# Kernel tuning notes

Hardware: AMD Instinct MI355X
Metric: run time of the kernel (lower is better)

## Reference

```python
import jax, jax.numpy as jnp
import numpy as np

UNITS = 32
OUT_STEPS = 24
B, T, F = 131072, 48, 1


def setup_inputs() -> dict:
    key = jax.random.key(0)
    ks = jax.random.split(key, 9)
    s = 0.1
    return {
        "inputs": jax.random.normal(ks[0], (B, T, F), jnp.float32),
        # warmup LSTM cell (inside lstm_rnn_warmup)
        "Wk_w": jax.random.normal(ks[1], (F, 4 * UNITS), jnp.float32) * s,
        "Uk_w": jax.random.normal(ks[2], (UNITS, 4 * UNITS), jnp.float32) * s,
        "b_w": jax.random.normal(ks[3], (4 * UNITS,), jnp.float32) * s,
        # decode LSTM cell (self.lstm_cell), input dim = 1 (prediction)
        "Wk_d": jax.random.normal(ks[4], (1, 4 * UNITS), jnp.float32) * s,
        "Uk_d": jax.random.normal(ks[5], (UNITS, 4 * UNITS), jnp.float32) * s,
        "b_d": jax.random.normal(ks[6], (4 * UNITS,), jnp.float32) * s,
        # dense projection to 1 output
        "Wd": jax.random.normal(ks[7], (UNITS, 1), jnp.float32) * s,
        "bd": jax.random.normal(ks[8], (1,), jnp.float32) * s,
    }


def _lstm_cell(x, h, c, Wk, Uk, b):
    # Keras LSTMCell: z = x@W + h@U + b ; split into i,f,g,o
    z = x @ Wk + h @ Uk + b
    i, f, g, o = jnp.split(z, 4, axis=-1)
    i = jax.nn.sigmoid(i)
    f = jax.nn.sigmoid(f)
    g = jnp.tanh(g)
    o = jax.nn.sigmoid(o)
    c_new = f * c + i * g
    h_new = o * jnp.tanh(c_new)
    return h_new, c_new


def reference(inputs, Wk_w, Uk_w, b_w, Wk_d, Uk_d, b_d, Wd, bd):
    b = inputs.shape[0]
    h0 = jnp.zeros((b, UNITS), inputs.dtype)
    c0 = jnp.zeros((b, UNITS), inputs.dtype)

    # warmup: run LSTM over input window, keep final state
    def warm_step(carry, x_t):
        h, c = carry
        h, c = _lstm_cell(x_t, h, c, Wk_w, Uk_w, b_w)
        return (h, c), None

    (h, c), _ = jax.lax.scan(warm_step, (h0, c0), jnp.swapaxes(inputs, 0, 1))
    pred = h @ Wd + bd  # [B, 1]

    def dec_step(carry, _):
        h, c, p = carry
        h, c = _lstm_cell(p, h, c, Wk_d, Uk_d, b_d)
        p = h @ Wd + bd
        return (h, c, p), p

    _, preds_rest = jax.lax.scan(dec_step, (h, c, pred), None, length=OUT_STEPS - 1)
    preds = jnp.concatenate([pred[None], preds_rest], axis=0)  # [S, B, 1]
    return jnp.transpose(preds, (1, 0, 2))  # [B, S, 1]
```

## Files before the change

kernel.cpp:

```cpp
#include <hip/hip_runtime.h>

#define TSTEPS 48
#define OUT_STEPS 24
#define L2E 1.44269504088896340736f
#define ECLAMP 30.0f

typedef short bf16x8 __attribute__((ext_vector_type(8)));
typedef float f32x16 __attribute__((ext_vector_type(16)));
typedef float f32x4 __attribute__((ext_vector_type(4)));
typedef unsigned int u32x4 __attribute__((ext_vector_type(4)));

__device__ __forceinline__ void bf_split_rne(float f, short& hi, short& lo) {
    unsigned u = __builtin_bit_cast(unsigned, f);
    unsigned r = u + 0x7FFFu + ((u >> 16) & 1u);
    unsigned short hb = (unsigned short)(r >> 16);
    float hif = __builtin_bit_cast(float, (unsigned)hb << 16);
    float lof = f - hif;
    unsigned short lb = (unsigned short)(__builtin_bit_cast(unsigned, lof) >> 16);
    hi = (short)hb; lo = (short)lb;
}

__device__ __forceinline__ float gate_scale(int g) {
    return (g == 2) ? (-2.0f * L2E) : (-L2E);
}

__device__ __forceinline__ int uslot(int cell, int g, int c) {
    return (cell * 4 + g) * 2 + c;
}

__device__ __forceinline__ void stage_a4(short* __restrict__ a4lds,
                                         const float* __restrict__ Wks,
                                         const float* __restrict__ bvs,
                                         int m, int H, int lane) {
#pragma unroll
    for (int g = 0; g < 4; ++g) {
        const float s = gate_scale(g);
        short whi, wlo, bhi, blo;
        bf_split_rne(Wks[g * 32 + m] * s, whi, wlo);
        bf_split_rne(bvs[g * 32 + m] * s, bhi, blo);
        bf16x8 a = {whi, wlo, bhi, blo, 0, 0, 0, 0};
        u32x4 z4 = {0u, 0u, 0u, 0u};
        if (H != 0) a = __builtin_bit_cast(bf16x8, z4);
        *(bf16x8*)(a4lds + (g * 64 + lane) * 8) = a;
    }
}

template <bool NEED_P>
__device__ __forceinline__ float lstm_step32(float x,
    const short* __restrict__ ufbase,
    const short* __restrict__ a4cell,
    u32x4& B0, u32x4& B1,
    float* cs, const float* __restrict__ wdp,
    int lane, unsigned hmask) {
    unsigned xr;
    asm("v_cvt_pk_bf16_f32 %0, %1, %2" : "=v"(xr) : "v"(x), "v"(x));
    unsigned w0 = xr & hmask;
    unsigned w1 = 0x3F803F80u & hmask;
    u32x4 b4u = {w0, w1, 0u, 0u};
    const bf16x8 B4 = __builtin_bit_cast(bf16x8, b4u);
    const bf16x8 b0 = __builtin_bit_cast(bf16x8, B0);
    const bf16x8 b1 = __builtin_bit_cast(bf16x8, B1);
    const f32x16 zero16 = {0,0,0,0,0,0,0,0,0,0,0,0,0,0,0,0};

    f32x16 acc[4];
#pragma unroll
    for (int g = 0; g < 4; ++g) {
        const bf16x8 A4g = *(const bf16x8*)(a4cell + (g * 64 + lane) * 8);
        const bf16x8 Ah0 = *(const bf16x8*)(ufbase + (uslot(0, g, 0) * 64 + lane) * 8);
        const bf16x8 Ah1 = *(const bf16x8*)(ufbase + (uslot(0, g, 1) * 64 + lane) * 8);
        f32x16 a = __builtin_amdgcn_mfma_f32_32x32x16_bf16(A4g, B4, zero16, 0, 0, 0);
        a = __builtin_amdgcn_mfma_f32_32x32x16_bf16(Ah0, b0, a, 0, 0, 0);
        a = __builtin_amdgcn_mfma_f32_32x32x16_bf16(Ah1, b1, a, 0, 0, 0);
        acc[g] = a;
    }

    float pp = 0.0f;
    float he = 0.0f;
    f32x4 wq = {0.0f, 0.0f, 0.0f, 0.0f};
#pragma unroll
    for (int r = 0; r < 16; ++r) {
        float ei = __builtin_amdgcn_exp2f(acc[0][r]);
        float ef = __builtin_amdgcn_exp2f(acc[1][r]);
        float eg = __builtin_amdgcn_exp2f(acc[2][r]);
        float eo = __builtin_amdgcn_exp2f(acc[3][r]);
        float di = 1.0f + ei, df = 1.0f + ef, dg = 1.0f + eg, do_ = 1.0f + eo;
        float ngs = __builtin_fmaf(eg, 2.0f * L2E, -2.0f * L2E);
        float t1 = di * dg;
        float t2 = cs[r] * t1;
        float num = __builtin_fmaf(ngs, df, t2);
        float cn = num * __builtin_amdgcn_rcpf(df * t1);
        cs[r] = cn;
        float ec = __builtin_amdgcn_exp2f(__builtin_fminf(cn, ECLAMP));
        float den = __builtin_fmaf(ec, do_, do_);
        float inv = __builtin_amdgcn_rcpf(den);
        float h = __builtin_fmaf(-ec, inv, inv);
        if constexpr (NEED_P) {
            if ((r & 3) == 0) wq = *(const f32x4*)(wdp + r);
            pp = __builtin_fmaf(h, wq[r & 3], pp);
        }
        if ((r & 1) == 0) {
            he = h;
        } else {
            unsigned d;
            asm("v_cvt_pk_bf16_f32 %0, %1, %2" : "=v"(d) : "v"(he), "v"(h));
            const int q = r >> 1;
            if (q < 4) B0[q] = d;
            else       B1[q - 4] = d;
        }
    }
    return pp;
}

__global__ __launch_bounds__(256, 4) void lstm_feedback_mfma22(
    const float* __restrict__ inputs,
    const float* __restrict__ Wk_w, const float* __restrict__ Uk_w, const float* __restrict__ b_w,
    const float* __restrict__ Wk_d, const float* __restrict__ Uk_d, const float* __restrict__ b_d,
    const float* __restrict__ Wd, const float* __restrict__ bd,
    float* __restrict__ out,
    int B) {
    const int tid = threadIdx.x;
    const int w = tid >> 6;
    const int lane = tid & 63;
    const int m = lane & 31;
    const int H = lane >> 5;
    const int mblk = blockIdx.x * 128;
    const long row = (long)(mblk + w * 32 + m);

    __shared__ __align__(16) short uflds[16 * 64 * 8];
    __shared__ __align__(16) short a4lds[4 * 64 * 8];
    __shared__ float wdlds[2][16];

    if (w < 2) {
        const float* Uks = w ? Uk_d : Uk_w;
#pragma unroll
        for (int g = 0; g < 4; ++g) {
            const float s = gate_scale(g);
#pragma unroll
            for (int c = 0; c < 2; ++c) {
                bf16x8 ah;
#pragma unroll
                for (int j = 0; j < 8; ++j) {
                    const int uin = 16 * c + 4 * H + (j & 3) + 8 * (j >> 2);
                    float wt = Uks[uin * 128 + g * 32 + m] * s;
                    short hb, lb; bf_split_rne(wt, hb, lb);
                    ah[j] = hb;
                }
                *(bf16x8*)(uflds + (uslot(w, g, c) * 64 + lane) * 8) = ah;
            }
        }
    }
    if (w == 0) stage_a4(a4lds, Wk_w, b_w, m, H, lane);
    if (tid < 32) {
        const int r = tid & 15, Hh = tid >> 4;
        wdlds[Hh][r] = Wd[(r & 3) + 8 * (r >> 2) + 4 * Hh];
    }

    const unsigned hmask = (H == 0) ? 0xFFFFFFFFu : 0u;

    u32x4 z4 = {0u, 0u, 0u, 0u};
    u32x4 B0 = z4, B1 = z4;
    float cs[16];
#pragma unroll
    for (int r = 0; r < 16; ++r) cs[r] = 0.0f;

    __syncthreads();

    const short* __restrict__ uf_w = uflds;
    const short* __restrict__ uf_d = uflds + 8 * 64 * 8;
    const float* __restrict__ wdp = &wdlds[H][0];

    float xc = inputs[row * TSTEPS + 0];
    for (int t = 0; t < TSTEPS - 1; ++t) {
        float xn = inputs[row * TSTEPS + t + 1];
        asm volatile("" ::: "memory");
        lstm_step32<false>(xc, uf_w, a4lds, B0, B1, cs, wdp, lane, hmask);
        xc = xn;
    }

    const float bdv = bd[0];

    asm volatile("" ::: "memory");
    float p = lstm_step32<true>(xc, uf_w, a4lds, B0, B1, cs, wdp, lane, hmask);
    p += __shfl_xor(p, 32);
    p += bdv;
    if (H == 0) out[row * OUT_STEPS + 0] = p;

    __syncthreads();
    if (w == 0) stage_a4(a4lds, Wk_d, b_d, m, H, lane);
    __syncthreads();

    for (int s = 1; s < OUT_STEPS; ++s) {
        asm volatile("" ::: "memory");
        p = lstm_step32<true>(p, uf_d, a4lds, B0, B1, cs, wdp, lane, hmask);
        p += __shfl_xor(p, 32);
        p += bdv;
        if (H == 0) out[row * OUT_STEPS + s] = p;
    }
}

extern "C" void kernel_launch(void* const* d_in, const int* in_sizes, int n_in,
                              void* d_out, int out_size, void* d_ws, size_t ws_size,
                              hipStream_t stream) {
    const float* inputs = (const float*)d_in[0];
    const float* Wk_w   = (const float*)d_in[1];
    const float* Uk_w   = (const float*)d_in[2];
    const float* b_w    = (const float*)d_in[3];
    const float* Wk_d   = (const float*)d_in[4];
    const float* Uk_d   = (const float*)d_in[5];
    const float* b_d    = (const float*)d_in[6];
    const float* Wd     = (const float*)d_in[7];
    const float* bd     = (const float*)d_in[8];
    float* out = (float*)d_out;

    const int B = in_sizes[0] / TSTEPS;
    const int grid = (B + 127) / 128;
    lstm_feedback_mfma22<<<grid, 256, 0, stream>>>(
        inputs, Wk_w, Uk_w, b_w, Wk_d, Uk_d, b_d, Wd, bd, out, B);
}
```

Measured before the change: 318.2 us.

## Keep LSTM weight fragments and Wd in registers instead of LDS

Loads the recurrent weight MFMA fragments, the input/bias fragment, and the dense-projection weights into per-thread registers once per phase, instead of re-reading them from shared memory every timestep. The launch bounds drop from 4 to 2 waves per SIMD so the extra registers fit, and the per-step compiler memory barriers are removed. This cuts per-step LDS read traffic and latency in exchange for fewer resident waves to hide MFMA and transcendental latency.

```diff
diff --git a/kernel.cpp b/kernel.cpp
--- a/kernel.cpp
+++ b/kernel.cpp
@@ -28,10 +28,9 @@
     return (cell * 4 + g) * 2 + c;
 }
 
-__device__ __forceinline__ void stage_a4(short* __restrict__ a4lds,
-                                         const float* __restrict__ Wks,
-                                         const float* __restrict__ bvs,
-                                         int m, int H, int lane) {
+__device__ __forceinline__ void make_a4(const float* __restrict__ Wks,
+                                        const float* __restrict__ bvs,
+                                        int m, int H, bf16x8* a4) {
 #pragma unroll
     for (int g = 0; g < 4; ++g) {
         const float s = gate_scale(g);
@@ -41,17 +40,18 @@
         bf16x8 a = {whi, wlo, bhi, blo, 0, 0, 0, 0};
         u32x4 z4 = {0u, 0u, 0u, 0u};
         if (H != 0) a = __builtin_bit_cast(bf16x8, z4);
-        *(bf16x8*)(a4lds + (g * 64 + lane) * 8) = a;
+        a4[g] = a;
     }
 }
 
 template <bool NEED_P>
 __device__ __forceinline__ float lstm_step32(float x,
-    const short* __restrict__ ufbase,
-    const short* __restrict__ a4cell,
+    const bf16x8* __restrict__ uf0,
+    const bf16x8* __restrict__ uf1,
+    const bf16x8* __restrict__ a4,
     u32x4& B0, u32x4& B1,
-    float* cs, const float* __restrict__ wdp,
-    int lane, unsigned hmask) {
+    float* cs, const f32x4* __restrict__ wq,
+    unsigned hmask) {
     unsigned xr;
     asm("v_cvt_pk_bf16_f32 %0, %1, %2" : "=v"(xr) : "v"(x), "v"(x));
     unsigned w0 = xr & hmask;
@@ -65,18 +65,14 @@
     f32x16 acc[4];
 #pragma unroll
     for (int g = 0; g < 4; ++g) {
-        const bf16x8 A4g = *(const bf16x8*)(a4cell + (g * 64 + lane) * 8);
-        const bf16x8 Ah0 = *(const bf16x8*)(ufbase + (uslot(0, g, 0) * 64 + lane) * 8);
-        const bf16x8 Ah1 = *(const bf16x8*)(ufbase + (uslot(0, g, 1) * 64 + lane) * 8);
-        f32x16 a = __builtin_amdgcn_mfma_f32_32x32x16_bf16(A4g, B4, zero16, 0, 0, 0);
-        a = __builtin_amdgcn_mfma_f32_32x32x16_bf16(Ah0, b0, a, 0, 0, 0);
-        a = __builtin_amdgcn_mfma_f32_32x32x16_bf16(Ah1, b1, a, 0, 0, 0);
+        f32x16 a = __builtin_amdgcn_mfma_f32_32x32x16_bf16(a4[g], B4, zero16, 0, 0, 0);
+        a = __builtin_amdgcn_mfma_f32_32x32x16_bf16(uf0[g], b0, a, 0, 0, 0);
+        a = __builtin_amdgcn_mfma_f32_32x32x16_bf16(uf1[g], b1, a, 0, 0, 0);
         acc[g] = a;
     }
 
     float pp = 0.0f;
     float he = 0.0f;
-    f32x4 wq = {0.0f, 0.0f, 0.0f, 0.0f};
 #pragma unroll
     for (int r = 0; r < 16; ++r) {
         float ei = __builtin_amdgcn_exp2f(acc[0][r]);
@@ -94,10 +90,7 @@
         float den = __builtin_fmaf(ec, do_, do_);
         float inv = __builtin_amdgcn_rcpf(den);
         float h = __builtin_fmaf(-ec, inv, inv);
-        if constexpr (NEED_P) {
-            if ((r & 3) == 0) wq = *(const f32x4*)(wdp + r);
-            pp = __builtin_fmaf(h, wq[r & 3], pp);
-        }
+        if constexpr (NEED_P) pp = __builtin_fmaf(h, wq[r >> 2][r & 3], pp);
         if ((r & 1) == 0) {
             he = h;
         } else {
@@ -111,7 +104,7 @@
     return pp;
 }
 
-__global__ __launch_bounds__(256, 4) void lstm_feedback_mfma22(
+__global__ __launch_bounds__(256, 2) void lstm_feedback_mfma23(
     const float* __restrict__ inputs,
     const float* __restrict__ Wk_w, const float* __restrict__ Uk_w, const float* __restrict__ b_w,
     const float* __restrict__ Wk_d, const float* __restrict__ Uk_d, const float* __restrict__ b_d,
@@ -127,8 +120,6 @@
     const long row = (long)(mblk + w * 32 + m);
 
     __shared__ __align__(16) short uflds[16 * 64 * 8];
-    __shared__ __align__(16) short a4lds[4 * 64 * 8];
-    __shared__ float wdlds[2][16];
 
     if (w < 2) {
         const float* Uks = w ? Uk_d : Uk_w;
@@ -149,13 +140,16 @@
             }
         }
     }
-    if (w == 0) stage_a4(a4lds, Wk_w, b_w, m, H, lane);
-    if (tid < 32) {
-        const int r = tid & 15, Hh = tid >> 4;
-        wdlds[Hh][r] = Wd[(r & 3) + 8 * (r >> 2) + 4 * Hh];
-    }
 
     const unsigned hmask = (H == 0) ? 0xFFFFFFFFu : 0u;
+
+    f32x4 wq[4];
+#pragma unroll
+    for (int r = 0; r < 16; ++r)
+        wq[r >> 2][r & 3] = Wd[(r & 3) + 8 * (r >> 2) + 4 * H];
+
+    bf16x8 a4[4];
+    make_a4(Wk_w, b_w, m, H, a4);
 
     u32x4 z4 = {0u, 0u, 0u, 0u};
     u32x4 B0 = z4, B1 = z4;
@@ -165,33 +159,36 @@
 
     __syncthreads();
 
-    const short* __restrict__ uf_w = uflds;
-    const short* __restrict__ uf_d = uflds + 8 * 64 * 8;
-    const float* __restrict__ wdp = &wdlds[H][0];
+    bf16x8 uf0[4], uf1[4];
+#pragma unroll
+    for (int g = 0; g < 4; ++g) {
+        uf0[g] = *(const bf16x8*)(uflds + (uslot(0, g, 0) * 64 + lane) * 8);
+        uf1[g] = *(const bf16x8*)(uflds + (uslot(0, g, 1) * 64 + lane) * 8);
+    }
 
     float xc = inputs[row * TSTEPS + 0];
     for (int t = 0; t < TSTEPS - 1; ++t) {
         float xn = inputs[row * TSTEPS + t + 1];
-        asm volatile("" ::: "memory");
-        lstm_step32<false>(xc, uf_w, a4lds, B0, B1, cs, wdp, lane, hmask);
+        lstm_step32<false>(xc, uf0, uf1, a4, B0, B1, cs, wq, hmask);
         xc = xn;
     }
 
     const float bdv = bd[0];
 
-    asm volatile("" ::: "memory");
-    float p = lstm_step32<true>(xc, uf_w, a4lds, B0, B1, cs, wdp, lane, hmask);
+    float p = lstm_step32<true>(xc, uf0, uf1, a4, B0, B1, cs, wq, hmask);
     p += __shfl_xor(p, 32);
     p += bdv;
     if (H == 0) out[row * OUT_STEPS + 0] = p;
 
-    __syncthreads();
-    if (w == 0) stage_a4(a4lds, Wk_d, b_d, m, H, lane);
-    __syncthreads();
+    make_a4(Wk_d, b_d, m, H, a4);
+#pragma unroll
+    for (int g = 0; g < 4; ++g) {
+        uf0[g] = *(const bf16x8*)(uflds + (uslot(1, g, 0) * 64 + lane) * 8);
+        uf1[g] = *(const bf16x8*)(uflds + (uslot(1, g, 1) * 64 + lane) * 8);
+    }
 
     for (int s = 1; s < OUT_STEPS; ++s) {
-        asm volatile("" ::: "memory");
-        p = lstm_step32<true>(p, uf_d, a4lds, B0, B1, cs, wdp, lane, hmask);
+        p = lstm_step32<true>(p, uf0, uf1, a4, B0, B1, cs, wq, hmask);
         p += __shfl_xor(p, 32);
         p += bdv;
         if (H == 0) out[row * OUT_STEPS + s] = p;
@@ -214,6 +211,6 @@
 
     const int B = in_sizes[0] / TSTEPS;
     const int grid = (B + 127) / 128;
-    lstm_feedback_mfma22<<<grid, 256, 0, stream>>>(
+    lstm_feedback_mfma23<<<grid, 256, 0, stream>>>(
         inputs, Wk_w, Uk_w, b_w, Wk_d, Uk_d, b_d, Wd, bd, out, B);
 }
```

New measurement: 311.7 us. 2.0% less time.
